# Kernel tuning notes

Measured on AMD Instinct MI355X. Metric: run time of the kernel, lower is better.

Reference implementation:

```python
import jax, jax.numpy as jnp
import numpy as np

B, N = 64, 196
D1, D2, H = 512, 2048, 512


def setup_inputs() -> dict:
    key = jax.random.key(0)
    ks = jax.random.split(key, 8)
    s1 = 1.0 / np.sqrt(D1)
    s2 = 1.0 / np.sqrt(D2)
    sh = 1.0 / np.sqrt(H)
    return {
        "input1": jax.random.normal(ks[0], (B, D1), jnp.float32),
        "input2": jax.random.normal(ks[1], (B, N, D2), jnp.float32),
        "W1": jax.random.uniform(ks[2], (D1, H), jnp.float32, -s1, s1),
        "b1": jax.random.uniform(ks[3], (H,), jnp.float32, -s1, s1),
        "W2": jax.random.uniform(ks[4], (D2, H), jnp.float32, -s2, s2),
        "b2": jax.random.uniform(ks[5], (H,), jnp.float32, -s2, s2),
        "Wf": jax.random.uniform(ks[6], (H, 1), jnp.float32, -sh, sh),
        "bf": jax.random.uniform(ks[7], (1,), jnp.float32, -sh, sh),
    }


def reference(input1, input2, W1, b1, W2, b2, Wf, bf):
    # enc1: [B, H]; enc2: [B, N, H]
    enc1 = input1 @ W1 + b1
    enc2 = jnp.einsum("bnd,dh->bnh", input2, W2) + b2
    # additive (Bahdanau) score: relu(enc2 + enc1[:,None]) @ Wf -> [B, N]
    scores = (jax.nn.relu(enc2 + enc1[:, None, :]) @ Wf)[..., 0] + bf[0]
    alpha = jax.nn.softmax(scores, axis=1)  # softmax over N regions
    att = jnp.einsum("bnd,bn->bd", input2, alpha)  # weighted sum of raw features
    return att, alpha
```

## Files before the change

kernel.cpp:

```cpp
#include <hip/hip_runtime.h>
#include <hip/hip_bf16.h>
#include <stdint.h>

#define BB 64
#define NN 196
#define D1c 512
#define D2c 2048
#define HHc 512
#define MM (BB*NN)

typedef __attribute__((ext_vector_type(8))) short bf16x8;
typedef __attribute__((ext_vector_type(4))) float f32x4;

__device__ inline ushort f2bf(float f){
  uint32_t u = __float_as_uint(f);
  u += 0x7fff + ((u >> 16) & 1);
  return (ushort)(u >> 16);
}
__device__ inline uint32_t pack2(float a, float b){
  return (uint32_t)f2bf(a) | ((uint32_t)f2bf(b) << 16);
}

__global__ __launch_bounds__(256) void w2t_kernel(const float* __restrict__ W2,
                                                  ushort* __restrict__ w2t){
  __shared__ float tile[64][65];
  const int ktb = blockIdx.x;
  const int ht  = blockIdx.y;
  const int t = threadIdx.x;
  const int tr = t >> 4;
  const int tc = (t & 15) * 4;
  #pragma unroll
  for (int p = 0; p < 4; ++p){
    int k = p*16 + tr;
    float4 v = *(const float4*)(W2 + (size_t)(ktb*64 + k)*HHc + ht*64 + tc);
    tile[k][tc] = v.x; tile[k][tc+1] = v.y; tile[k][tc+2] = v.z; tile[k][tc+3] = v.w;
  }
  __syncthreads();
  #pragma unroll
  for (int pp = 0; pp < 4; ++pp){
    int hl = pp*16 + tr;
    ushort4 o;
    o.x = f2bf(tile[tc  ][hl]);
    o.y = f2bf(tile[tc+1][hl]);
    o.z = f2bf(tile[tc+2][hl]);
    o.w = f2bf(tile[tc+3][hl]);
    size_t addr = (size_t)(ht*4 + pp)*32768 + (size_t)ktb*1024
                + (size_t)((tc>>5)&1)*512 + (size_t)((tc>>3)&3)*128
                + (size_t)tr*8 + (tc & 4);
    *(ushort4*)(w2t + addr) = o;
  }
}

__global__ __launch_bounds__(128) void enc1_kernel(const float* __restrict__ in1,
                                                   const float* __restrict__ W1,
                                                   const float* __restrict__ b1,
                                                   float* __restrict__ enc1){
  __shared__ float s1[D1c];
  const int b = blockIdx.x;
  const int ht = blockIdx.y;
  const int t = threadIdx.x;
  ((float4*)s1)[t] = ((const float4*)(in1 + (size_t)b*D1c))[t];
  __syncthreads();
  const int h = ht*128 + t;
  float acc = b1[h];
  #pragma unroll 8
  for (int d = 0; d < D1c; ++d)
    acc += s1[d] * W1[(size_t)d*HHc + h];
  enc1[b*HHc + h] = acc;
}

__global__ __launch_bounds__(256) void score_gemm(
    const float*  __restrict__ in2,
    const ushort* __restrict__ w2t,
    const float*  __restrict__ b2,
    const float*  __restrict__ wf,
    const float*  __restrict__ enc1,
    float*        __restrict__ scores)
{
  __shared__ ushort As[2][64*64];

  const int t = threadIdx.x;
  const int p  = blockIdx.x;
  const int lg = (p & 7) * 49 + (p >> 3);
  const int h0 = (lg & 1) * 256;
  const int m0 = (lg >> 1) * 64;

  const int wave = t >> 6, lane = t & 63;
  const int l15 = lane & 15, l4 = lane >> 4;

  const int arow = t >> 2;
  const int aq   = t & 3;
  const float* aBase = in2 + (size_t)(m0 + arow)*D2c + aq*16;
  const int ac0 = ((aq*2    ) ^ (arow & 7)) << 3;
  const int ac1 = ((aq*2 + 1) ^ (arow & 7)) << 3;

  const ushort* bBase = w2t + (size_t)h0*2048 + (size_t)wave*131072 + lane*8;

  float b2v[4], wfv[4];
  #pragma unroll
  for (int hf = 0; hf < 4; ++hf){
    int hc = h0 + wave*64 + hf*16 + l15;
    b2v[hf] = b2[hc]; wfv[hf] = wf[hc];
  }

  f32x4 acc[4][4];
  #pragma unroll
  for (int i = 0; i < 4; ++i)
    #pragma unroll
    for (int j = 0; j < 4; ++j) acc[i][j] = (f32x4)0.f;

  float4 aReg[4];
  bf16x8 bA[8], bB[8];

#define A_LOAD(kt)                                                           \
  { _Pragma("unroll")                                                        \
    for (int j = 0; j < 4; ++j)                                              \
      aReg[j] = *(const float4*)(aBase + (kt)*64 + j*4); }

#define B_LOAD(kt, B)                                                        \
  { _Pragma("unroll")                                                        \
    for (int f = 0; f < 8; ++f)                                              \
      B[f] = *(const bf16x8*)(bBase + (f>>1)*32768 + (kt)*1024 + (f&1)*512); }

#define A_WRITE(buf)                                                         \
  { uint4 w0, w1;                                                            \
    w0.x = pack2(aReg[0].x, aReg[0].y); w0.y = pack2(aReg[0].z, aReg[0].w);  \
    w0.z = pack2(aReg[1].x, aReg[1].y); w0.w = pack2(aReg[1].z, aReg[1].w);  \
    w1.x = pack2(aReg[2].x, aReg[2].y); w1.y = pack2(aReg[2].z, aReg[2].w);  \
    w1.z = pack2(aReg[3].x, aReg[3].y); w1.w = pack2(aReg[3].z, aReg[3].w);  \
    *(uint4*)(As[buf] + arow*64 + ac0) = w0;                                 \
    *(uint4*)(As[buf] + arow*64 + ac1) = w1; }

#define COMPUTE(buf, B)                                                      \
  { _Pragma("unroll")                                                        \
    for (int kk = 0; kk < 2; ++kk){                                          \
      bf16x8 af[4];                                                          \
      _Pragma("unroll")                                                      \
      for (int mf = 0; mf < 4; ++mf){                                        \
        int r = mf*16 + l15, c = kk*4 + l4;                                  \
        af[mf] = *(const bf16x8*)(As[buf] + r*64 + ((c ^ (r & 7)) << 3)); }  \
      _Pragma("unroll")                                                      \
      for (int mf = 0; mf < 4; ++mf)                                         \
        _Pragma("unroll")                                                    \
        for (int hf = 0; hf < 4; ++hf)                                       \
          acc[mf][hf] = __builtin_amdgcn_mfma_f32_16x16x32_bf16(             \
              af[mf], B[hf*2+kk], acc[mf][hf], 0, 0, 0); } }

#define LGKM0() asm volatile("s_waitcnt lgkmcnt(0)" ::: "memory")
#define SB0()   __builtin_amdgcn_sched_barrier(0)
#define BAR()   { SB0(); __builtin_amdgcn_s_barrier(); SB0(); }

  A_LOAD(0);
  B_LOAD(0, bA);
  A_WRITE(0);
  LGKM0();
  BAR();

  #pragma unroll 1
  for (int kt = 0; kt < 30; kt += 2){
    A_LOAD(kt + 1);
    B_LOAD(kt + 1, bB);
    COMPUTE(0, bA);
    A_WRITE(1);
    LGKM0();
    BAR();
    A_LOAD(kt + 2);
    B_LOAD(kt + 2, bA);
    COMPUTE(1, bB);
    A_WRITE(0);
    LGKM0();
    BAR();
  }
  A_LOAD(31);
  B_LOAD(31, bB);
  COMPUTE(0, bA);
  A_WRITE(1);
  LGKM0();
  BAR();
  COMPUTE(1, bB);

  #pragma unroll
  for (int mf = 0; mf < 4; ++mf){
    #pragma unroll
    for (int r = 0; r < 4; ++r){
      int m = m0 + mf*16 + l4*4 + r;
      int b = m / NN;
      const float* e1 = enc1 + (size_t)b*HHc + h0 + wave*64 + l15;
      float s = 0.f;
      #pragma unroll
      for (int hf = 0; hf < 4; ++hf){
        float v = acc[mf][hf][r] + b2v[hf] + e1[hf*16];
        s += fmaxf(v, 0.f) * wfv[hf];
      }
      s += __shfl_xor(s, 1); s += __shfl_xor(s, 2);
      s += __shfl_xor(s, 4); s += __shfl_xor(s, 8);
      if (l15 == 0) atomicAdd(&scores[m], s);
    }
  }
#undef A_LOAD
#undef B_LOAD
#undef A_WRITE
#undef COMPUTE
#undef LGKM0
#undef SB0
#undef BAR
}

__global__ __launch_bounds__(64) void softmax_kernel(const float* __restrict__ scores,
                                                     float* __restrict__ alpha){
  const int b = blockIdx.x, t = threadIdx.x;
  const float* s = scores + b*NN;
  float x[4]; float mx = -1e30f;
  #pragma unroll
  for (int i = 0; i < 4; ++i){
    int n = t + i*64;
    x[i] = (n < NN) ? s[n] : -1e30f;
    mx = fmaxf(mx, x[i]);
  }
  #pragma unroll
  for (int o = 1; o < 64; o <<= 1) mx = fmaxf(mx, __shfl_xor(mx, o));
  float sum = 0.f;
  #pragma unroll
  for (int i = 0; i < 4; ++i){
    int n = t + i*64;
    float e = (n < NN) ? __expf(x[i] - mx) : 0.f;
    x[i] = e; sum += e;
  }
  #pragma unroll
  for (int o = 1; o < 64; o <<= 1) sum += __shfl_xor(sum, o);
  float inv = 1.f / sum;
  #pragma unroll
  for (int i = 0; i < 4; ++i){
    int n = t + i*64;
    if (n < NN) alpha[b*NN + n] = x[i] * inv;
  }
}

__global__ __launch_bounds__(256) void att_kernel(const float* __restrict__ in2,
                                                  const float* __restrict__ alpha,
                                                  float* __restrict__ att){
  __shared__ float sal[NN];
  const int b = blockIdx.y;
  const int t = threadIdx.x;
  if (t < NN) sal[t] = alpha[b*NN + t];
  __syncthreads();
  const int d = blockIdx.x*256 + t;
  const float* src = in2 + (size_t)b*NN*D2c + d;
  float acc = 0.f;
  #pragma unroll 7
  for (int n = 0; n < NN; ++n)
    acc += src[(size_t)n*D2c] * sal[n];
  att[(size_t)b*D2c + d] = acc;
}

extern "C" void kernel_launch(void* const* d_in, const int* in_sizes, int n_in,
                              void* d_out, int out_size, void* d_ws, size_t ws_size,
                              hipStream_t stream){
  (void)in_sizes; (void)n_in; (void)out_size; (void)ws_size;
  const float* input1 = (const float*)d_in[0];
  const float* input2 = (const float*)d_in[1];
  const float* W1     = (const float*)d_in[2];
  const float* b1     = (const float*)d_in[3];
  const float* W2     = (const float*)d_in[4];
  const float* b2     = (const float*)d_in[5];
  const float* Wf     = (const float*)d_in[6];

  float* out   = (float*)d_out;
  float* att   = out;
  float* alpha = out + BB*D2c;

  char*   ws     = (char*)d_ws;
  ushort* w2t    = (ushort*)ws;
  float*  enc1   = (float*)(ws + 2*1024*1024);
  float*  scores = (float*)(ws + 2*1024*1024 + 131072);

  hipMemsetAsync(scores, 0, MM*sizeof(float), stream);
  w2t_kernel<<<dim3(32, 8), 256, 0, stream>>>(W2, w2t);
  enc1_kernel<<<dim3(BB, 4), 128, 0, stream>>>(input1, W1, b1, enc1);
  score_gemm<<<dim3(392), 256, 0, stream>>>(input2, w2t, b2, Wf, enc1, scores);
  softmax_kernel<<<dim3(BB), 64, 0, stream>>>(scores, alpha);
  att_kernel<<<dim3(8, BB), 256, 0, stream>>>(input2, alpha, att);
}
```

Before: 105.3 us.

## Halve score GEMM H-tile, double grid, prefetch A two stages ahead, use hardware bf16 convert

The score GEMM now uses 64x128 tiles instead of 64x256, doubling the grid to 784 blocks and halving accumulator and B-register use so three blocks can share a CU. The A-operand global loads are issued two k-steps ahead using two register sets, giving more latency hiding. The software bf16 rounding is replaced with the v_cvt_pk_bf16_f32 instruction. The trade-off is that the fp32 input2 rows are read and converted twice as often (four H tiles instead of two), which raises memory traffic.

```diff
diff --git a/kernel.cpp b/kernel.cpp
--- a/kernel.cpp
+++ b/kernel.cpp
@@ -17,8 +17,10 @@
   u += 0x7fff + ((u >> 16) & 1);
   return (ushort)(u >> 16);
 }
-__device__ inline uint32_t pack2(float a, float b){
-  return (uint32_t)f2bf(a) | ((uint32_t)f2bf(b) << 16);
+__device__ inline uint32_t cvtpk(float lo, float hi){
+  uint32_t r;
+  asm("v_cvt_pk_bf16_f32 %0, %1, %2" : "=v"(r) : "v"(lo), "v"(hi));
+  return r;
 }
 
 __global__ __launch_bounds__(256) void w2t_kernel(const float* __restrict__ W2,
@@ -69,7 +71,7 @@
   enc1[b*HHc + h] = acc;
 }
 
-__global__ __launch_bounds__(256) void score_gemm(
+__global__ __launch_bounds__(256,3) void score_gemm(
     const float*  __restrict__ in2,
     const ushort* __restrict__ w2t,
     const float*  __restrict__ b2,
@@ -81,9 +83,9 @@
 
   const int t = threadIdx.x;
   const int p  = blockIdx.x;
-  const int lg = (p & 7) * 49 + (p >> 3);
-  const int h0 = (lg & 1) * 256;
-  const int m0 = (lg >> 1) * 64;
+  const int lg = (p & 7) * 98 + (p >> 3);
+  const int h0 = (lg & 3) * 128;
+  const int m0 = (lg >> 2) * 64;
 
   const int wave = t >> 6, lane = t & 63;
   const int l15 = lane & 15, l4 = lane >> 4;
@@ -94,44 +96,44 @@
   const int ac0 = ((aq*2    ) ^ (arow & 7)) << 3;
   const int ac1 = ((aq*2 + 1) ^ (arow & 7)) << 3;
 
-  const ushort* bBase = w2t + (size_t)h0*2048 + (size_t)wave*131072 + lane*8;
-
-  float b2v[4], wfv[4];
-  #pragma unroll
-  for (int hf = 0; hf < 4; ++hf){
-    int hc = h0 + wave*64 + hf*16 + l15;
+  const ushort* bBase = w2t + (size_t)h0*2048 + (size_t)wave*65536 + lane*8;
+
+  float b2v[2], wfv[2];
+  #pragma unroll
+  for (int hf = 0; hf < 2; ++hf){
+    int hc = h0 + wave*32 + hf*16 + l15;
     b2v[hf] = b2[hc]; wfv[hf] = wf[hc];
   }
 
-  f32x4 acc[4][4];
+  f32x4 acc[4][2];
   #pragma unroll
   for (int i = 0; i < 4; ++i)
     #pragma unroll
-    for (int j = 0; j < 4; ++j) acc[i][j] = (f32x4)0.f;
-
-  float4 aReg[4];
-  bf16x8 bA[8], bB[8];
-
-#define A_LOAD(kt)                                                           \
+    for (int j = 0; j < 2; ++j) acc[i][j] = (f32x4)0.f;
+
+  float4 aRegA[4], aRegB[4];
+  bf16x8 bRegA[4], bRegB[4];
+
+#define A_LOAD(kt, R)                                                        \
   { _Pragma("unroll")                                                        \
     for (int j = 0; j < 4; ++j)                                              \
-      aReg[j] = *(const float4*)(aBase + (kt)*64 + j*4); }
-
-#define B_LOAD(kt, B)                                                        \
+      R[j] = *(const float4*)(aBase + (kt)*64 + j*4); }
+
+#define B_LOAD(kt, Bv)                                                       \
   { _Pragma("unroll")                                                        \
-    for (int f = 0; f < 8; ++f)                                              \
-      B[f] = *(const bf16x8*)(bBase + (f>>1)*32768 + (kt)*1024 + (f&1)*512); }
-
-#define A_WRITE(buf)                                                         \
+    for (int f = 0; f < 4; ++f)                                              \
+      Bv[f] = *(const bf16x8*)(bBase + (f>>1)*32768 + (kt)*1024 + (f&1)*512); }
+
+#define A_WRITE(R, buf)                                                      \
   { uint4 w0, w1;                                                            \
-    w0.x = pack2(aReg[0].x, aReg[0].y); w0.y = pack2(aReg[0].z, aReg[0].w);  \
-    w0.z = pack2(aReg[1].x, aReg[1].y); w0.w = pack2(aReg[1].z, aReg[1].w);  \
-    w1.x = pack2(aReg[2].x, aReg[2].y); w1.y = pack2(aReg[2].z, aReg[2].w);  \
-    w1.z = pack2(aReg[3].x, aReg[3].y); w1.w = pack2(aReg[3].z, aReg[3].w);  \
+    w0.x = cvtpk(R[0].x, R[0].y); w0.y = cvtpk(R[0].z, R[0].w);              \
+    w0.z = cvtpk(R[1].x, R[1].y); w0.w = cvtpk(R[1].z, R[1].w);              \
+    w1.x = cvtpk(R[2].x, R[2].y); w1.y = cvtpk(R[2].z, R[2].w);              \
+    w1.z = cvtpk(R[3].x, R[3].y); w1.w = cvtpk(R[3].z, R[3].w);              \
     *(uint4*)(As[buf] + arow*64 + ac0) = w0;                                 \
     *(uint4*)(As[buf] + arow*64 + ac1) = w1; }
 
-#define COMPUTE(buf, B)                                                      \
+#define COMPUTE(buf, Bv)                                                     \
   { _Pragma("unroll")                                                        \
     for (int kk = 0; kk < 2; ++kk){                                          \
       bf16x8 af[4];                                                          \
@@ -142,42 +144,42 @@
       _Pragma("unroll")                                                      \
       for (int mf = 0; mf < 4; ++mf)                                         \
         _Pragma("unroll")                                                    \
-        for (int hf = 0; hf < 4; ++hf)                                       \
+        for (int hf = 0; hf < 2; ++hf)                                       \
           acc[mf][hf] = __builtin_amdgcn_mfma_f32_16x16x32_bf16(             \
-              af[mf], B[hf*2+kk], acc[mf][hf], 0, 0, 0); } }
+              af[mf], Bv[hf*2+kk], acc[mf][hf], 0, 0, 0); } }
 
 #define LGKM0() asm volatile("s_waitcnt lgkmcnt(0)" ::: "memory")
 #define SB0()   __builtin_amdgcn_sched_barrier(0)
 #define BAR()   { SB0(); __builtin_amdgcn_s_barrier(); SB0(); }
 
-  A_LOAD(0);
-  B_LOAD(0, bA);
-  A_WRITE(0);
+  A_LOAD(0, aRegA);
+  B_LOAD(0, bRegA);
+  A_LOAD(1, aRegB);
+  A_WRITE(aRegA, 0);
   LGKM0();
   BAR();
 
   #pragma unroll 1
   for (int kt = 0; kt < 30; kt += 2){
-    A_LOAD(kt + 1);
-    B_LOAD(kt + 1, bB);
-    COMPUTE(0, bA);
-    A_WRITE(1);
+    B_LOAD(kt + 1, bRegB);
+    A_LOAD(kt + 2, aRegA);
+    COMPUTE(0, bRegA);
+    A_WRITE(aRegB, 1);
     LGKM0();
     BAR();
-    A_LOAD(kt + 2);
-    B_LOAD(kt + 2, bA);
-    COMPUTE(1, bB);
-    A_WRITE(0);
+    B_LOAD(kt + 2, bRegA);
+    A_LOAD(kt + 3, aRegB);
+    COMPUTE(1, bRegB);
+    A_WRITE(aRegA, 0);
     LGKM0();
     BAR();
   }
-  A_LOAD(31);
-  B_LOAD(31, bB);
-  COMPUTE(0, bA);
-  A_WRITE(1);
+  B_LOAD(31, bRegB);
+  COMPUTE(0, bRegA);
+  A_WRITE(aRegB, 1);
   LGKM0();
   BAR();
-  COMPUTE(1, bB);
+  COMPUTE(1, bRegB);
 
   #pragma unroll
   for (int mf = 0; mf < 4; ++mf){
@@ -185,10 +187,10 @@
     for (int r = 0; r < 4; ++r){
       int m = m0 + mf*16 + l4*4 + r;
       int b = m / NN;
-      const float* e1 = enc1 + (size_t)b*HHc + h0 + wave*64 + l15;
+      const float* e1 = enc1 + (size_t)b*HHc + h0 + wave*32 + l15;
       float s = 0.f;
       #pragma unroll
-      for (int hf = 0; hf < 4; ++hf){
+      for (int hf = 0; hf < 2; ++hf){
         float v = acc[mf][hf][r] + b2v[hf] + e1[hf*16];
         s += fmaxf(v, 0.f) * wfv[hf];
       }
@@ -277,7 +279,7 @@
   hipMemsetAsync(scores, 0, MM*sizeof(float), stream);
   w2t_kernel<<<dim3(32, 8), 256, 0, stream>>>(W2, w2t);
   enc1_kernel<<<dim3(BB, 4), 128, 0, stream>>>(input1, W1, b1, enc1);
-  score_gemm<<<dim3(392), 256, 0, stream>>>(input2, w2t, b2, Wf, enc1, scores);
+  score_gemm<<<dim3(784), 256, 0, stream>>>(input2, w2t, b2, Wf, enc1, scores);
   softmax_kernel<<<dim3(BB), 64, 0, stream>>>(scores, alpha);
   att_kernel<<<dim3(8, BB), 256, 0, stream>>>(input2, alpha, att);
 }
```

Measured after the change: 112.3 us. 1.07x slower.
